# Optimization experiments

Hardware: AMD Instinct MI355X
Metric: run time of the kernel (lower is better)

The kernel has to match this reference:

```python
import jax, jax.numpy as jnp
import numpy as np

N = 100000
E = 3200000
IN_DIM = 64
HID = 64
G = 4096
BN_EPS = 1e-5


def setup_inputs() -> dict:
    key = jax.random.key(0)
    ks = jax.random.split(key, 20)
    def lin(k, fi, fo):
        bound = 1.0 / np.sqrt(fi)
        kw, kb = jax.random.split(k)
        W = jax.random.uniform(kw, (fi, fo), jnp.float32, -bound, bound)
        b = jax.random.uniform(kb, (fo,), jnp.float32, -bound, bound)
        return W, b
    x = jax.random.normal(ks[0], (N, IN_DIM), jnp.float32)
    edge_index = jax.random.randint(ks[1], (2, E), 0, N, jnp.int64)
    batch = jnp.sort(jax.random.randint(ks[2], (N,), 0, G, jnp.int64))
    proj_W, proj_b = lin(ks[3], IN_DIM, HID)
    conv1_W, conv1_b = lin(ks[4], HID, HID)
    conv2_W, conv2_b = lin(ks[5], HID, HID)
    conv3_W, conv3_b = lin(ks[6], HID, HID)
    head_W1, head_b1 = lin(ks[7], HID, HID // 2)
    head_W2, head_b2 = lin(ks[8], HID // 2, 1)
    ones = jnp.ones((HID,), jnp.float32)
    zeros = jnp.zeros((HID,), jnp.float32)
    return dict(
        x=x, edge_index=edge_index, batch=batch,
        proj_W=proj_W, proj_b=proj_b,
        conv1_W=conv1_W, conv1_b=conv1_b,
        conv2_W=conv2_W, conv2_b=conv2_b,
        conv3_W=conv3_W, conv3_b=conv3_b,
        bn1_g=ones, bn1_b=zeros, bn2_g=ones, bn2_b=zeros,
        bn3_g=ones, bn3_b=zeros,
        head_W1=head_W1, head_b1=head_b1,
        head_W2=head_W2, head_b2=head_b2,
    )


def _gcn_conv(x, W, b, src, dst, dinv):
    # GCNConv with self-loops and symmetric normalization (PyG semantics).
    xl = x @ W                                   # [N, H]
    norm = dinv[src] * dinv[dst]                 # [E]
    msg = xl[src] * norm[:, None]                # [E, H]  (memory-bound gather)
    agg = jax.ops.segment_sum(msg, dst, num_segments=x.shape[0])
    agg = agg + (dinv * dinv)[:, None] * xl      # self-loop contribution
    return agg + b


def _bn(h, g, b):
    mu = jnp.mean(h, axis=0)
    var = jnp.var(h, axis=0)
    return (h - mu) * jax.lax.rsqrt(var + BN_EPS) * g + b


def reference(x, edge_index, batch,
              proj_W, proj_b,
              conv1_W, conv1_b, conv2_W, conv2_b, conv3_W, conv3_b,
              bn1_g, bn1_b, bn2_g, bn2_b, bn3_g, bn3_b,
              head_W1, head_b1, head_W2, head_b2):
    src, dst = edge_index[0], edge_index[1]
    n = x.shape[0]
    # degree including self loop
    deg = jax.ops.segment_sum(jnp.ones_like(dst, jnp.float32), dst, num_segments=n) + 1.0
    dinv = jax.lax.rsqrt(deg)

    x0 = jax.nn.relu(x @ proj_W + proj_b)
    h = jax.nn.relu(_bn(_gcn_conv(x0, conv1_W, conv1_b, src, dst, dinv), bn1_g, bn1_b))
    h = jax.nn.relu(_bn(_gcn_conv(h, conv2_W, conv2_b, src, dst, dinv), bn2_g, bn2_b))
    h = h + x0
    h = jax.nn.relu(_bn(_gcn_conv(h, conv3_W, conv3_b, src, dst, dinv), bn3_g, bn3_b))

    # global mean pool over graphs
    sums = jax.ops.segment_sum(h, batch, num_segments=G)
    cnts = jax.ops.segment_sum(jnp.ones((n,), jnp.float32), batch, num_segments=G)
    pooled = sums / jnp.maximum(cnts, 1.0)[:, None]

    out = jax.nn.relu(pooled @ head_W1 + head_b1) @ head_W2 + head_b2
    return out.squeeze(-1)
```

## Files before the change

kernel.cpp:

```cpp
#include <hip/hip_runtime.h>
#include <hip/hip_fp16.h>

#define NNODES 100000
#define NEDGES 3200000
#define NGRAPH 4096
#define SBCNT 196
#define SBCAP 17504
#define P1CHUNK 4096
#define P1CAP 56
#define P1GRID 782
#define AGG_GRID 1563
#define BN_EPS 1e-5f
#define INV_N (1.0f / 100000.0f)

__global__ void k_zero_i(int* __restrict__ p, int n) {
  int i = blockIdx.x * blockDim.x + threadIdx.x;
  int st = gridDim.x * blockDim.x;
  for (; i < n; i += st) p[i] = 0;
}
__global__ void k_zero_f(float* __restrict__ p, int n) {
  int i = blockIdx.x * blockDim.x + threadIdx.x;
  int st = gridDim.x * blockDim.x;
  for (; i < n; i += st) p[i] = 0.0f;
}

__global__ void k_part1(const int* __restrict__ src, const int* __restrict__ dst,
                        int* __restrict__ sbcur, int* __restrict__ sbbuf, int e) {
  __shared__ int cnt[SBCNT];
  __shared__ int base[SBCNT];
  __shared__ int bins[SBCNT * P1CAP];
  int t = threadIdx.x;
  int start = blockIdx.x * P1CHUNK;
  int end = min(start + P1CHUNK, e);
  for (int i = t; i < SBCNT; i += 256) cnt[i] = 0;
  __syncthreads();
  for (int i = start + t; i < end; i += 256) {
    int s = src[i], d = dst[i];
    int sb = d >> 9;
    int en = (s << 9) | (d & 511);
    int pos = atomicAdd(&cnt[sb], 1);
    if (pos < P1CAP) {
      bins[sb * P1CAP + pos] = en;
    } else {
      int gp = atomicAdd(&sbcur[sb], 1);
      if (gp < SBCAP) sbbuf[(size_t)sb * SBCAP + gp] = en;
    }
  }
  __syncthreads();
  if (t < SBCNT) {
    int c = min(cnt[t], P1CAP);
    base[t] = (c > 0) ? atomicAdd(&sbcur[t], c) : 0;
  }
  __syncthreads();
  int lane = t & 63, wid = t >> 6;
  for (int b = wid; b < SBCNT; b += 4) {
    int c = min(cnt[b], P1CAP);
    if (lane < c) {
      int gp = base[b] + lane;
      if (gp < SBCAP) sbbuf[(size_t)b * SBCAP + gp] = bins[b * P1CAP + lane];
    }
  }
}

__global__ void k_part2(const int* __restrict__ sbcur, const int* __restrict__ sbbuf,
                        int* __restrict__ slots, int* __restrict__ deg,
                        int* __restrict__ rowstart) {
  __shared__ int cnt[512];
  __shared__ int pfx[512];
  __shared__ int cur[512];
  int sb = blockIdx.x;
  int t = threadIdx.x;
  int n = min(sbcur[sb], SBCAP);
  const int* __restrict__ pb = sbbuf + (size_t)sb * SBCAP;
  cnt[t] = 0;
  __syncthreads();
  for (int i = t; i < n; i += 512) atomicAdd(&cnt[pb[i] & 511], 1);
  __syncthreads();
  int myc = cnt[t];
  pfx[t] = myc;
  __syncthreads();
  for (int o = 1; o < 512; o <<= 1) {
    int x = (t >= o) ? pfx[t - o] : 0;
    __syncthreads();
    pfx[t] += x;
    __syncthreads();
  }
  int excl = pfx[t] - myc;
  int node = sb * 512 + t;
  if (node < NNODES) {
    deg[node] = myc;
    rowstart[node] = sb * SBCAP + excl;
  }
  cur[t] = 0;
  __syncthreads();
  pfx[t] = excl;
  __syncthreads();
  for (int i = t; i < n; i += 512) {
    int e = pb[i];
    int dl = e & 511;
    int pos = atomicAdd(&cur[dl], 1);
    slots[(size_t)sb * SBCAP + pfx[dl] + pos] = e >> 9;
  }
}

__global__ void k_dinv(const int* __restrict__ deg, float* __restrict__ dinv, int n) {
  int i = blockIdx.x * blockDim.x + threadIdx.x;
  if (i < n) dinv[i] = rsqrtf((float)deg[i] + 1.0f);
}

template <int PRO, bool EPI_DINV, bool EPI_BR>
__global__ void k_gemm64(const float* __restrict__ A, const float* __restrict__ W,
                         const float* __restrict__ bias, const float* __restrict__ stats,
                         const float* __restrict__ g, const float* __restrict__ bb,
                         const float* __restrict__ res, const float* __restrict__ dinv,
                         float* __restrict__ C, __half* __restrict__ Ch, int n) {
  __shared__ float Ws[64 * 64];
  __shared__ float As[64 * 64];
  __shared__ float scs[64], shs[64], bs[64];
  int t = threadIdx.x;
  {
    const float4* W4 = (const float4*)W;
    float4* Ws4 = (float4*)Ws;
    for (int i = t; i < 1024; i += 256) Ws4[i] = W4[i];
  }
  if (t < 64) {
    if (EPI_BR) bs[t] = bias[t];
    if (PRO >= 1) {
      float mu = stats[t] * INV_N;
      float var = stats[64 + t] * INV_N - mu * mu;
      float sc = g[t] * rsqrtf(var + BN_EPS);
      scs[t] = sc;
      shs[t] = bb[t] - mu * sc;
    }
  }
  int row0 = blockIdx.x * 64;
  int rows = min(64, n - row0);
  __syncthreads();
  {
    const float4* A4 = (const float4*)(A + (size_t)row0 * 64);
    const float4* R4 = (PRO == 2) ? (const float4*)(res + (size_t)row0 * 64) : nullptr;
    float4* As4 = (float4*)As;
    for (int i = t; i < rows * 16; i += 256) {
      float4 v = A4[i];
      if (PRO >= 1) {
        int c0 = (i & 15) * 4;
        v.x = fmaxf(fmaf(v.x, scs[c0], shs[c0]), 0.0f);
        v.y = fmaxf(fmaf(v.y, scs[c0 + 1], shs[c0 + 1]), 0.0f);
        v.z = fmaxf(fmaf(v.z, scs[c0 + 2], shs[c0 + 2]), 0.0f);
        v.w = fmaxf(fmaf(v.w, scs[c0 + 3], shs[c0 + 3]), 0.0f);
        if (PRO == 2) {
          float4 r4 = R4[i];
          v.x += r4.x; v.y += r4.y; v.z += r4.z; v.w += r4.w;
        }
      }
      As4[i] = v;
    }
  }
  __syncthreads();
  int c = t & 63;
  int w = t >> 6;
  float acc[16];
#pragma unroll
  for (int j = 0; j < 16; ++j) acc[j] = 0.0f;
#pragma unroll 4
  for (int k = 0; k < 64; ++k) {
    float wv = Ws[(k << 6) + c];
#pragma unroll
    for (int j = 0; j < 16; ++j) {
      acc[j] = fmaf(As[((w + 4 * j) << 6) + k], wv, acc[j]);
    }
  }
#pragma unroll
  for (int j = 0; j < 16; ++j) {
    int r = w + 4 * j;
    if (r < rows) {
      float o = acc[j];
      if (EPI_BR) o = fmaxf(o + bs[c], 0.0f);
      if (EPI_DINV) {
        o *= dinv[row0 + r];
        Ch[(size_t)(row0 + r) * 64 + c] = __float2half(o);
      } else {
        C[(size_t)(row0 + r) * 64 + c] = o;
      }
    }
  }
}

__global__ void k_agg(const int* __restrict__ deg, const int* __restrict__ rowstart,
                      const int* __restrict__ slots, const __half* __restrict__ y,
                      const float* __restrict__ dinv, float* __restrict__ ag,
                      float* __restrict__ pstats) {
  int t = threadIdx.x;
  int lane = t & 63, wid = t >> 6;
  int wave = blockIdx.x * 4 + wid;
  int nw = gridDim.x * 4;
  float s = 0.0f, q = 0.0f;
  for (int node0 = wave; node0 < NNODES; node0 += nw) {
    int node = __builtin_amdgcn_readfirstlane(node0);
    int m = deg[node];
    const int* __restrict__ sp = slots + rowstart[node];
    float a0 = __half2float(y[(size_t)node * 64 + lane]);
    float a1 = 0.0f, a2 = 0.0f, a3 = 0.0f;
    float a4 = 0.0f, a5 = 0.0f, a6 = 0.0f, a7 = 0.0f;
    int k = 0;
    for (; k + 16 <= m; k += 16) {
      int s0 = sp[k + 0],  s1 = sp[k + 1],  s2 = sp[k + 2],  s3 = sp[k + 3];
      int s4 = sp[k + 4],  s5 = sp[k + 5],  s6 = sp[k + 6],  s7 = sp[k + 7];
      int s8 = sp[k + 8],  s9 = sp[k + 9],  sa = sp[k + 10], sb = sp[k + 11];
      int sc = sp[k + 12], sd = sp[k + 13], se = sp[k + 14], sf = sp[k + 15];
      __half v0 = y[(size_t)s0 * 64 + lane];
      __half v1 = y[(size_t)s1 * 64 + lane];
      __half v2 = y[(size_t)s2 * 64 + lane];
      __half v3 = y[(size_t)s3 * 64 + lane];
      __half v4 = y[(size_t)s4 * 64 + lane];
      __half v5 = y[(size_t)s5 * 64 + lane];
      __half v6 = y[(size_t)s6 * 64 + lane];
      __half v7 = y[(size_t)s7 * 64 + lane];
      __half v8 = y[(size_t)s8 * 64 + lane];
      __half v9 = y[(size_t)s9 * 64 + lane];
      __half va = y[(size_t)sa * 64 + lane];
      __half vb = y[(size_t)sb * 64 + lane];
      __half vc = y[(size_t)sc * 64 + lane];
      __half vd = y[(size_t)sd * 64 + lane];
      __half ve = y[(size_t)se * 64 + lane];
      __half vf = y[(size_t)sf * 64 + lane];
      a0 += __half2float(v0); a1 += __half2float(v1);
      a2 += __half2float(v2); a3 += __half2float(v3);
      a4 += __half2float(v4); a5 += __half2float(v5);
      a6 += __half2float(v6); a7 += __half2float(v7);
      a0 += __half2float(v8); a1 += __half2float(v9);
      a2 += __half2float(va); a3 += __half2float(vb);
      a4 += __half2float(vc); a5 += __half2float(vd);
      a6 += __half2float(ve); a7 += __half2float(vf);
    }
    for (; k + 4 <= m; k += 4) {
      int s0 = sp[k + 0], s1 = sp[k + 1], s2 = sp[k + 2], s3 = sp[k + 3];
      __half v0 = y[(size_t)s0 * 64 + lane];
      __half v1 = y[(size_t)s1 * 64 + lane];
      __half v2 = y[(size_t)s2 * 64 + lane];
      __half v3 = y[(size_t)s3 * 64 + lane];
      a0 += __half2float(v0); a1 += __half2float(v1);
      a2 += __half2float(v2); a3 += __half2float(v3);
    }
    for (; k < m; ++k) a0 += __half2float(y[(size_t)sp[k] * 64 + lane]);
    float o = dinv[node] * (((a0 + a1) + (a2 + a3)) + ((a4 + a5) + (a6 + a7)));
    ag[(size_t)node0 * 64 + lane] = o;
    s += o;
    q = fmaf(o, o, q);
  }
  __shared__ float ls[256], lq[256];
  ls[t] = s;
  lq[t] = q;
  __syncthreads();
  if (t < 64) {
    pstats[blockIdx.x * 128 + t] = ls[t] + ls[64 + t] + ls[128 + t] + ls[192 + t];
    pstats[blockIdx.x * 128 + 64 + t] = lq[t] + lq[64 + t] + lq[128 + t] + lq[192 + t];
  }
}

__global__ void k_stats_reduce(const float* __restrict__ pstats, float* __restrict__ stats) {
  __shared__ float red[256];
  int c = blockIdx.x;
  int t = threadIdx.x;
  float s = 0.0f;
  for (int i = t; i < AGG_GRID; i += 256) s += pstats[i * 128 + c];
  red[t] = s;
  __syncthreads();
  for (int o = 128; o >= 1; o >>= 1) {
    if (t < o) red[t] += red[t + o];
    __syncthreads();
  }
  if (t == 0) stats[c] = red[0];
}

__global__ void k_pool(const float* __restrict__ ag, const float* __restrict__ stats,
                       const float* __restrict__ g, const float* __restrict__ bb,
                       const int* __restrict__ batch, float* __restrict__ psum,
                       float* __restrict__ pcnt) {
  int t = threadIdx.x, lane = t & 63;
  int wave = blockIdx.x * 4 + (t >> 6);
  int c0 = wave * 32;
  if (c0 >= NNODES) return;
  float mu = stats[lane] * INV_N;
  float var = stats[64 + lane] * INV_N - mu * mu;
  float sc = g[lane] * rsqrtf(var + BN_EPS);
  float sh = bb[lane] - mu * sc;
  int gprev = -1;
  float av = 0.0f, cv = 0.0f;
  int end = min(c0 + 32, NNODES);
  for (int node = c0; node < end; ++node) {
    int gi = batch[node];
    if (gi != gprev) {
      if (gprev >= 0) {
        atomicAdd(&psum[gprev * 64 + lane], av);
        if (lane == 0) atomicAdd(&pcnt[gprev], cv);
      }
      gprev = gi;
      av = 0.0f;
      cv = 0.0f;
    }
    av += fmaxf(fmaf(ag[(size_t)node * 64 + lane], sc, sh), 0.0f);
    cv += 1.0f;
  }
  if (gprev >= 0) {
    atomicAdd(&psum[gprev * 64 + lane], av);
    if (lane == 0) atomicAdd(&pcnt[gprev], cv);
  }
}

__global__ void k_head(const float* __restrict__ psum, const float* __restrict__ pcnt,
                       const float* __restrict__ W1, const float* __restrict__ b1,
                       const float* __restrict__ W2, const float* __restrict__ b2,
                       float* __restrict__ out) {
  int gidx = blockIdx.x;
  int t = threadIdx.x;
  __shared__ float pooled[64];
  __shared__ float hid[32];
  float cnt = fmaxf(pcnt[gidx], 1.0f);
  pooled[t] = psum[gidx * 64 + t] / cnt;
  __syncthreads();
  if (t < 32) {
    float a = b1[t];
#pragma unroll
    for (int k = 0; k < 64; ++k) a = fmaf(pooled[k], W1[k * 32 + t], a);
    hid[t] = fmaxf(a, 0.0f);
  }
  __syncthreads();
  if (t == 0) {
    float o = b2[0];
#pragma unroll
    for (int j = 0; j < 32; ++j) o = fmaf(hid[j], W2[j], o);
    out[gidx] = o;
  }
}

extern "C" void kernel_launch(void* const* d_in, const int* in_sizes, int n_in,
                              void* d_out, int out_size, void* d_ws, size_t ws_size,
                              hipStream_t stream) {
  const float* x       = (const float*)d_in[0];
  const int*   eidx    = (const int*)d_in[1];
  const int*   batch   = (const int*)d_in[2];
  const float* proj_W  = (const float*)d_in[3];
  const float* proj_b  = (const float*)d_in[4];
  const float* conv1_W = (const float*)d_in[5];
  const float* conv2_W = (const float*)d_in[7];
  const float* conv3_W = (const float*)d_in[9];
  const float* bn1_g   = (const float*)d_in[11];
  const float* bn1_b   = (const float*)d_in[12];
  const float* bn2_g   = (const float*)d_in[13];
  const float* bn2_b   = (const float*)d_in[14];
  const float* bn3_g   = (const float*)d_in[15];
  const float* bn3_b   = (const float*)d_in[16];
  const float* head_W1 = (const float*)d_in[17];
  const float* head_b1 = (const float*)d_in[18];
  const float* head_W2 = (const float*)d_in[19];
  const float* head_b2 = (const float*)d_in[20];
  float* out = (float*)d_out;

  const int N = NNODES, E = NEDGES, G = NGRAPH;
  const int* src = eidx;
  const int* dst = eidx + E;

  char* p = (char*)d_ws;
  auto align256 = [](size_t v) { return (v + 255) & ~(size_t)255; };
  int* sbcur = (int*)p;      p += align256((size_t)SBCNT * 4);
  int* deg = (int*)p;        p += align256((size_t)N * 4);
  int* rowstart = (int*)p;   p += align256((size_t)N * 4);
  int* slots = (int*)p;      p += align256((size_t)SBCNT * SBCAP * 4);
  float* dinv = (float*)p;   p += align256((size_t)N * 4);
  float* x0 = (float*)p;     p += align256((size_t)N * 64 * 4);
  __half* y16 = (__half*)p;  p += align256((size_t)N * 64 * 2);
  float* ag = (float*)p;     p += align256((size_t)N * 64 * 4);
  float* pstats = (float*)p; p += align256((size_t)AGG_GRID * 128 * 4);
  float* stats1 = (float*)p; p += align256(128 * 4);
  float* stats2 = (float*)p; p += align256(128 * 4);
  float* stats3 = (float*)p; p += align256(128 * 4);
  float* psum = (float*)p;   p += align256((size_t)G * 64 * 4);
  float* pcnt = (float*)p;   p += align256((size_t)G * 4);
  int* sbbuf = (int*)x0;

  const int TB = 256;
  int gemm_grid = (N + 63) / 64;

  k_zero_i<<<1, SBCNT, 0, stream>>>(sbcur, SBCNT);
  k_part1<<<P1GRID, TB, 0, stream>>>(src, dst, sbcur, sbbuf, E);
  k_part2<<<SBCNT, 512, 0, stream>>>(sbcur, sbbuf, slots, deg, rowstart);
  k_dinv<<<(N + TB - 1) / TB, TB, 0, stream>>>(deg, dinv, N);

  k_zero_f<<<(G * 64 + G + TB - 1) / TB, TB, 0, stream>>>(psum, G * 64 + G);

  k_gemm64<0, false, true><<<gemm_grid, TB, 0, stream>>>(
      x, proj_W, proj_b, nullptr, nullptr, nullptr, nullptr, nullptr, x0, nullptr, N);

  k_gemm64<0, true, false><<<gemm_grid, TB, 0, stream>>>(
      x0, conv1_W, nullptr, nullptr, nullptr, nullptr, nullptr, dinv, nullptr, y16, N);
  k_agg<<<AGG_GRID, TB, 0, stream>>>(deg, rowstart, slots, y16, dinv, ag, pstats);
  k_stats_reduce<<<128, TB, 0, stream>>>(pstats, stats1);

  k_gemm64<1, true, false><<<gemm_grid, TB, 0, stream>>>(
      ag, conv2_W, nullptr, stats1, bn1_g, bn1_b, nullptr, dinv, nullptr, y16, N);
  k_agg<<<AGG_GRID, TB, 0, stream>>>(deg, rowstart, slots, y16, dinv, ag, pstats);
  k_stats_reduce<<<128, TB, 0, stream>>>(pstats, stats2);

  k_gemm64<2, true, false><<<gemm_grid, TB, 0, stream>>>(
      ag, conv3_W, nullptr, stats2, bn2_g, bn2_b, x0, dinv, nullptr, y16, N);
  k_agg<<<AGG_GRID, TB, 0, stream>>>(deg, rowstart, slots, y16, dinv, ag, pstats);
  k_stats_reduce<<<128, TB, 0, stream>>>(pstats, stats3);

  k_pool<<<(N + 127) / 128, TB, 0, stream>>>(ag, stats3, bn3_g, bn3_b, batch, psum, pcnt);
  k_head<<<G, 64, 0, stream>>>(psum, pcnt, head_W1, head_b1, head_W2, head_b2, out);
}
```

Before: 422.3 us.

## Gather half2 per lane with two neighbors per wave in GCN aggregation

```diff
diff --git a/kernel.cpp b/kernel.cpp
--- a/kernel.cpp
+++ b/kernel.cpp
@@ -64,7 +64,7 @@
 
 __global__ void k_part2(const int* __restrict__ sbcur, const int* __restrict__ sbbuf,
                         int* __restrict__ slots, int* __restrict__ deg,
-                        int* __restrict__ rowstart) {
+                        int* __restrict__ rowstart, float* __restrict__ dinv) {
   __shared__ int cnt[512];
   __shared__ int pfx[512];
   __shared__ int cur[512];
@@ -90,6 +90,7 @@
   if (node < NNODES) {
     deg[node] = myc;
     rowstart[node] = sb * SBCAP + excl;
+    dinv[node] = rsqrtf((float)myc + 1.0f);
   }
   cur[t] = 0;
   __syncthreads();
@@ -101,11 +102,6 @@
     int pos = atomicAdd(&cur[dl], 1);
     slots[(size_t)sb * SBCAP + pfx[dl] + pos] = e >> 9;
   }
-}
-
-__global__ void k_dinv(const int* __restrict__ deg, float* __restrict__ dinv, int n) {
-  int i = blockIdx.x * blockDim.x + threadIdx.x;
-  if (i < n) dinv[i] = rsqrtf((float)deg[i] + 1.0f);
 }
 
 template <int PRO, bool EPI_DINV, bool EPI_BR>
@@ -187,74 +183,132 @@
 }
 
 __global__ void k_agg(const int* __restrict__ deg, const int* __restrict__ rowstart,
-                      const int* __restrict__ slots, const __half* __restrict__ y,
+                      const int* __restrict__ slots, const __half2* __restrict__ y2,
                       const float* __restrict__ dinv, float* __restrict__ ag,
                       float* __restrict__ pstats) {
   int t = threadIdx.x;
   int lane = t & 63, wid = t >> 6;
+  int cp = lane & 31;
+  int hp = lane >> 5;
   int wave = blockIdx.x * 4 + wid;
   int nw = gridDim.x * 4;
-  float s = 0.0f, q = 0.0f;
+  float sx = 0.0f, sy = 0.0f, qx = 0.0f, qy = 0.0f;
   for (int node0 = wave; node0 < NNODES; node0 += nw) {
     int node = __builtin_amdgcn_readfirstlane(node0);
     int m = deg[node];
     const int* __restrict__ sp = slots + rowstart[node];
-    float a0 = __half2float(y[(size_t)node * 64 + lane]);
-    float a1 = 0.0f, a2 = 0.0f, a3 = 0.0f;
-    float a4 = 0.0f, a5 = 0.0f, a6 = 0.0f, a7 = 0.0f;
+    float a0x = 0, a0y = 0, a1x = 0, a1y = 0, a2x = 0, a2y = 0, a3x = 0, a3y = 0;
+    float a4x = 0, a4y = 0, a5x = 0, a5y = 0, a6x = 0, a6y = 0, a7x = 0, a7y = 0;
+    if (hp == 0) {
+      float2 f = __half22float2(y2[(size_t)node * 32 + cp]);
+      a0x += f.x; a0y += f.y;
+    }
     int k = 0;
-    for (; k + 16 <= m; k += 16) {
-      int s0 = sp[k + 0],  s1 = sp[k + 1],  s2 = sp[k + 2],  s3 = sp[k + 3];
-      int s4 = sp[k + 4],  s5 = sp[k + 5],  s6 = sp[k + 6],  s7 = sp[k + 7];
-      int s8 = sp[k + 8],  s9 = sp[k + 9],  sa = sp[k + 10], sb = sp[k + 11];
-      int sc = sp[k + 12], sd = sp[k + 13], se = sp[k + 14], sf = sp[k + 15];
-      __half v0 = y[(size_t)s0 * 64 + lane];
-      __half v1 = y[(size_t)s1 * 64 + lane];
-      __half v2 = y[(size_t)s2 * 64 + lane];
-      __half v3 = y[(size_t)s3 * 64 + lane];
-      __half v4 = y[(size_t)s4 * 64 + lane];
-      __half v5 = y[(size_t)s5 * 64 + lane];
-      __half v6 = y[(size_t)s6 * 64 + lane];
-      __half v7 = y[(size_t)s7 * 64 + lane];
-      __half v8 = y[(size_t)s8 * 64 + lane];
-      __half v9 = y[(size_t)s9 * 64 + lane];
-      __half va = y[(size_t)sa * 64 + lane];
-      __half vb = y[(size_t)sb * 64 + lane];
-      __half vc = y[(size_t)sc * 64 + lane];
-      __half vd = y[(size_t)sd * 64 + lane];
-      __half ve = y[(size_t)se * 64 + lane];
-      __half vf = y[(size_t)sf * 64 + lane];
-      a0 += __half2float(v0); a1 += __half2float(v1);
-      a2 += __half2float(v2); a3 += __half2float(v3);
-      a4 += __half2float(v4); a5 += __half2float(v5);
-      a6 += __half2float(v6); a7 += __half2float(v7);
-      a0 += __half2float(v8); a1 += __half2float(v9);
-      a2 += __half2float(va); a3 += __half2float(vb);
-      a4 += __half2float(vc); a5 += __half2float(vd);
-      a6 += __half2float(ve); a7 += __half2float(vf);
-    }
-    for (; k + 4 <= m; k += 4) {
-      int s0 = sp[k + 0], s1 = sp[k + 1], s2 = sp[k + 2], s3 = sp[k + 3];
-      __half v0 = y[(size_t)s0 * 64 + lane];
-      __half v1 = y[(size_t)s1 * 64 + lane];
-      __half v2 = y[(size_t)s2 * 64 + lane];
-      __half v3 = y[(size_t)s3 * 64 + lane];
-      a0 += __half2float(v0); a1 += __half2float(v1);
-      a2 += __half2float(v2); a3 += __half2float(v3);
-    }
-    for (; k < m; ++k) a0 += __half2float(y[(size_t)sp[k] * 64 + lane]);
-    float o = dinv[node] * (((a0 + a1) + (a2 + a3)) + ((a4 + a5) + (a6 + a7)));
-    ag[(size_t)node0 * 64 + lane] = o;
-    s += o;
-    q = fmaf(o, o, q);
-  }
-  __shared__ float ls[256], lq[256];
-  ls[t] = s;
-  lq[t] = q;
+    for (; k + 32 <= m; k += 32) {
+      int i0 = hp ? sp[k + 1] : sp[k + 0];
+      int i1 = hp ? sp[k + 3] : sp[k + 2];
+      int i2 = hp ? sp[k + 5] : sp[k + 4];
+      int i3 = hp ? sp[k + 7] : sp[k + 6];
+      int i4 = hp ? sp[k + 9] : sp[k + 8];
+      int i5 = hp ? sp[k + 11] : sp[k + 10];
+      int i6 = hp ? sp[k + 13] : sp[k + 12];
+      int i7 = hp ? sp[k + 15] : sp[k + 14];
+      int i8 = hp ? sp[k + 17] : sp[k + 16];
+      int i9 = hp ? sp[k + 19] : sp[k + 18];
+      int ia = hp ? sp[k + 21] : sp[k + 20];
+      int ib = hp ? sp[k + 23] : sp[k + 22];
+      int ic = hp ? sp[k + 25] : sp[k + 24];
+      int id = hp ? sp[k + 27] : sp[k + 26];
+      int ie = hp ? sp[k + 29] : sp[k + 28];
+      int if_ = hp ? sp[k + 31] : sp[k + 30];
+      __half2 v0 = y2[(size_t)i0 * 32 + cp];
+      __half2 v1 = y2[(size_t)i1 * 32 + cp];
+      __half2 v2 = y2[(size_t)i2 * 32 + cp];
+      __half2 v3 = y2[(size_t)i3 * 32 + cp];
+      __half2 v4 = y2[(size_t)i4 * 32 + cp];
+      __half2 v5 = y2[(size_t)i5 * 32 + cp];
+      __half2 v6 = y2[(size_t)i6 * 32 + cp];
+      __half2 v7 = y2[(size_t)i7 * 32 + cp];
+      __half2 v8 = y2[(size_t)i8 * 32 + cp];
+      __half2 v9 = y2[(size_t)i9 * 32 + cp];
+      __half2 va = y2[(size_t)ia * 32 + cp];
+      __half2 vb = y2[(size_t)ib * 32 + cp];
+      __half2 vc = y2[(size_t)ic * 32 + cp];
+      __half2 vd = y2[(size_t)id * 32 + cp];
+      __half2 ve = y2[(size_t)ie * 32 + cp];
+      __half2 vf = y2[(size_t)if_ * 32 + cp];
+      float2 f;
+      f = __half22float2(v0); a0x += f.x; a0y += f.y;
+      f = __half22float2(v1); a1x += f.x; a1y += f.y;
+      f = __half22float2(v2); a2x += f.x; a2y += f.y;
+      f = __half22float2(v3); a3x += f.x; a3y += f.y;
+      f = __half22float2(v4); a4x += f.x; a4y += f.y;
+      f = __half22float2(v5); a5x += f.x; a5y += f.y;
+      f = __half22float2(v6); a6x += f.x; a6y += f.y;
+      f = __half22float2(v7); a7x += f.x; a7y += f.y;
+      f = __half22float2(v8); a0x += f.x; a0y += f.y;
+      f = __half22float2(v9); a1x += f.x; a1y += f.y;
+      f = __half22float2(va); a2x += f.x; a2y += f.y;
+      f = __half22float2(vb); a3x += f.x; a3y += f.y;
+      f = __half22float2(vc); a4x += f.x; a4y += f.y;
+      f = __half22float2(vd); a5x += f.x; a5y += f.y;
+      f = __half22float2(ve); a6x += f.x; a6y += f.y;
+      f = __half22float2(vf); a7x += f.x; a7y += f.y;
+    }
+    for (; k + 8 <= m; k += 8) {
+      int i0 = hp ? sp[k + 1] : sp[k + 0];
+      int i1 = hp ? sp[k + 3] : sp[k + 2];
+      int i2 = hp ? sp[k + 5] : sp[k + 4];
+      int i3 = hp ? sp[k + 7] : sp[k + 6];
+      __half2 v0 = y2[(size_t)i0 * 32 + cp];
+      __half2 v1 = y2[(size_t)i1 * 32 + cp];
+      __half2 v2 = y2[(size_t)i2 * 32 + cp];
+      __half2 v3 = y2[(size_t)i3 * 32 + cp];
+      float2 f;
+      f = __half22float2(v0); a0x += f.x; a0y += f.y;
+      f = __half22float2(v1); a1x += f.x; a1y += f.y;
+      f = __half22float2(v2); a2x += f.x; a2y += f.y;
+      f = __half22float2(v3); a3x += f.x; a3y += f.y;
+    }
+    for (; k + 2 <= m; k += 2) {
+      int i0 = hp ? sp[k + 1] : sp[k + 0];
+      float2 f = __half22float2(y2[(size_t)i0 * 32 + cp]);
+      a0x += f.x; a0y += f.y;
+    }
+    if (k < m && hp == 0) {
+      float2 f = __half22float2(y2[(size_t)sp[k] * 32 + cp]);
+      a0x += f.x; a0y += f.y;
+    }
+    float atx = ((a0x + a1x) + (a2x + a3x)) + ((a4x + a5x) + (a6x + a7x));
+    float aty = ((a0y + a1y) + (a2y + a3y)) + ((a4y + a5y) + (a6y + a7y));
+    float totx = atx + __shfl_xor(atx, 32);
+    float toty = aty + __shfl_xor(aty, 32);
+    float dv = dinv[node];
+    float ox = dv * totx;
+    float oy = dv * toty;
+    if (hp == 0) {
+      float2 o2; o2.x = ox; o2.y = oy;
+      ((float2*)ag)[(size_t)node0 * 32 + cp] = o2;
+      sx += ox; sy += oy;
+      qx = fmaf(ox, ox, qx); qy = fmaf(oy, oy, qy);
+    }
+  }
+  __shared__ float lsx[128], lsy[128], lqx[128], lqy[128];
+  if (hp == 0) {
+    int idx = wid * 32 + cp;
+    lsx[idx] = sx; lsy[idx] = sy; lqx[idx] = qx; lqy[idx] = qy;
+  }
   __syncthreads();
   if (t < 64) {
-    pstats[blockIdx.x * 128 + t] = ls[t] + ls[64 + t] + ls[128 + t] + ls[192 + t];
-    pstats[blockIdx.x * 128 + 64 + t] = lq[t] + lq[64 + t] + lq[128 + t] + lq[192 + t];
+    int cpp = t >> 1, comp = t & 1;
+    float S = 0.0f, Q = 0.0f;
+#pragma unroll
+    for (int w = 0; w < 4; ++w) {
+      S += comp ? lsy[w * 32 + cpp] : lsx[w * 32 + cpp];
+      Q += comp ? lqy[w * 32 + cpp] : lqx[w * 32 + cpp];
+    }
+    pstats[blockIdx.x * 128 + t] = S;
+    pstats[blockIdx.x * 128 + 64 + t] = Q;
   }
 }
 
@@ -384,8 +438,7 @@
 
   k_zero_i<<<1, SBCNT, 0, stream>>>(sbcur, SBCNT);
   k_part1<<<P1GRID, TB, 0, stream>>>(src, dst, sbcur, sbbuf, E);
-  k_part2<<<SBCNT, 512, 0, stream>>>(sbcur, sbbuf, slots, deg, rowstart);
-  k_dinv<<<(N + TB - 1) / TB, TB, 0, stream>>>(deg, dinv, N);
+  k_part2<<<SBCNT, 512, 0, stream>>>(sbcur, sbbuf, slots, deg, rowstart, dinv);
 
   k_zero_f<<<(G * 64 + G + TB - 1) / TB, TB, 0, stream>>>(psum, G * 64 + G);
 
@@ -394,17 +447,17 @@
 
   k_gemm64<0, true, false><<<gemm_grid, TB, 0, stream>>>(
       x0, conv1_W, nullptr, nullptr, nullptr, nullptr, nullptr, dinv, nullptr, y16, N);
-  k_agg<<<AGG_GRID, TB, 0, stream>>>(deg, rowstart, slots, y16, dinv, ag, pstats);
+  k_agg<<<AGG_GRID, TB, 0, stream>>>(deg, rowstart, slots, (const __half2*)y16, dinv, ag, pstats);
   k_stats_reduce<<<128, TB, 0, stream>>>(pstats, stats1);
 
   k_gemm64<1, true, false><<<gemm_grid, TB, 0, stream>>>(
       ag, conv2_W, nullptr, stats1, bn1_g, bn1_b, nullptr, dinv, nullptr, y16, N);
-  k_agg<<<AGG_GRID, TB, 0, stream>>>(deg, rowstart, slots, y16, dinv, ag, pstats);
+  k_agg<<<AGG_GRID, TB, 0, stream>>>(deg, rowstart, slots, (const __half2*)y16, dinv, ag, pstats);
   k_stats_reduce<<<128, TB, 0, stream>>>(pstats, stats2);
 
   k_gemm64<2, true, false><<<gemm_grid, TB, 0, stream>>>(
       ag, conv3_W, nullptr, stats2, bn2_g, bn2_b, x0, dinv, nullptr, y16, N);
-  k_agg<<<AGG_GRID, TB, 0, stream>>>(deg, rowstart, slots, y16, dinv, ag, pstats);
+  k_agg<<<AGG_GRID, TB, 0, stream>>>(deg, rowstart, slots, (const __half2*)y16, dinv, ag, pstats);
   k_stats_reduce<<<128, TB, 0, stream>>>(pstats, stats3);
 
   k_pool<<<(N + 127) / 128, TB, 0, stream>>>(ag, stats3, bn3_g, bn3_b, batch, psum, pcnt);
```

After: 571.3 us. 1.35x slower.
